# Performance work log

Hardware: AMD Instinct MI355X
Metric: run time of the kernel (lower is better)

Reference implementation:

```python
import jax, jax.numpy as jnp
import numpy as np

H_IMG, W_IMG = 32, 32   # image_size -> seq_len = 1024
NH, HD, D = 8, 32, 256  # num_heads, head_dim, d_model
B = 8


def _relative_positions(h, w):
    # Swin-style relative position index table, [h*w, h*w] int32
    y = np.arange(h); x = np.arange(w)
    coords = np.stack(np.meshgrid(y, x, indexing='ij')).reshape(2, -1)  # [2, S]
    rel = coords[:, :, None] - coords[:, None, :]                      # [2, S, S]
    rel = rel.transpose(1, 2, 0).astype(np.int64)                      # [S, S, 2]
    rel[:, :, 0] += h - 1
    rel[:, :, 1] += w - 1
    rel[:, :, 0] *= 2 * w - 1
    return np.int32(rel.sum(-1))                                       # [S, S]

_POS = _relative_positions(H_IMG, W_IMG)


def setup_inputs() -> dict:
    key = jax.random.key(0)
    ks = jax.random.split(key, 8)
    S = H_IMG * W_IMG
    return {
        'inputs_q': jax.random.normal(ks[0], (B, S, D), jnp.float32),
        'inputs_kv': jax.random.normal(ks[1], (B, S, D), jnp.float32),
        'Wq': jax.random.normal(ks[2], (D, NH, HD), jnp.float32) / np.sqrt(D),
        'bq': jnp.zeros((NH, HD), jnp.float32),
        'Wk': jax.random.normal(ks[3], (D, NH, HD), jnp.float32) / np.sqrt(D),
        'bk': jnp.zeros((NH, HD), jnp.float32),
        'Wv': jax.random.normal(ks[4], (D, NH, HD), jnp.float32) / np.sqrt(D),
        'bv': jnp.zeros((NH, HD), jnp.float32),
        'rel_table': 0.02 * jax.random.normal(ks[5], ((2 * H_IMG - 1) * (2 * W_IMG - 1), NH), jnp.float32),
        'Wo': jax.random.normal(ks[6], (NH, HD, D), jnp.float32) / np.sqrt(NH * HD),
        'bo': jnp.zeros((D,), jnp.float32),
    }


def reference(inputs_q, inputs_kv, Wq, bq, Wk, bk, Wv, bv, rel_table, Wo, bo):
    pos = jnp.asarray(_POS)                                  # [S, S] int32 (constant)
    q = jnp.einsum('bsd,dhk->bshk', inputs_q, Wq) + bq       # [B, S, H, HD]
    k = jnp.einsum('bsd,dhk->bshk', inputs_kv, Wk) + bk
    v = jnp.einsum('bsd,dhk->bshk', inputs_kv, Wv) + bv
    q = q / jnp.sqrt(jnp.asarray(HD, q.dtype))
    attn = jnp.einsum('bqhd,bkhd->bhqk', q, k)               # [B, H, S, S]
    rel_bias = rel_table[pos]                                # [S, S, H]
    attn = attn + jnp.transpose(rel_bias, (2, 0, 1))[None]   # broadcast over batch
    attn = jax.nn.softmax(attn, axis=-1)
    x = jnp.einsum('bhqk,bkhd->bqhd', attn, v)               # [B, S, H, HD]
    return jnp.einsum('bqhd,hdf->bqf', x, Wo) + bo           # [B, S, D]
```

## Files before the change

### kernel.cpp

```cpp
#include <hip/hip_runtime.h>

#define B_SZ   8
#define S_LEN  1024
#define D_MOD  256
#define NHEADS 8
#define M_ROWS 8192
#define LOG2E  1.4426950408889634f
#define QSCALE_LOG2E 0.2550352766751165f

typedef _Float16 f16x8 __attribute__((ext_vector_type(8)));
typedef _Float16 f16x4 __attribute__((ext_vector_type(4)));
typedef float    f32x4 __attribute__((ext_vector_type(4)));

__global__ __launch_bounds__(256)
void prep_kernel(const float* __restrict__ Wq, const float* __restrict__ Wk,
                 const float* __restrict__ Wv, const float* __restrict__ Wo,
                 const float* __restrict__ rel,
                 _Float16* __restrict__ wtp, float* __restrict__ tab) {
    if (blockIdx.x < 32) {
        __shared__ _Float16 Wl[32 * 264];
        const int mi = blockIdx.x >> 3;
        const int k0 = (blockIdx.x & 7) << 5;
        const float* W = (mi == 0) ? Wq : (mi == 1) ? Wk : (mi == 2) ? Wv : Wo;
        {
            const int r  = threadIdx.x >> 3;
            const int c4 = (threadIdx.x & 7) * 4;
            const float* src = W + (size_t)(k0 + r) * 256 + c4;
#pragma unroll
            for (int g = 0; g < 8; ++g) {
                f32x4 v = *(const f32x4*)(src + g * 32);
                f16x4 o;
#pragma unroll
                for (int j = 0; j < 4; ++j) o[j] = (_Float16)v[j];
                *(f16x4*)(&Wl[r * 264 + c4 + g * 32]) = o;
            }
        }
        __syncthreads();
        const int n16 = threadIdx.x >> 4;
        const int l16 = threadIdx.x & 15;
        const int kk  = k0 >> 5;
#pragma unroll
        for (int quad = 0; quad < 4; ++quad) {
            f16x8 v;
#pragma unroll
            for (int j = 0; j < 8; ++j) v[j] = Wl[(quad * 8 + j) * 264 + n16 * 16 + l16];
            *(f16x8*)(wtp + (((size_t)(mi * 16 + n16) * 8 + kk) << 9) + (quad * 16 + l16) * 8) = v;
        }
        return;
    }
    __shared__ float rl[63 * 8];
    const int dy31 = blockIdx.x - 32;
    for (int f = threadIdx.x; f < 504; f += 256) rl[f] = rel[(size_t)dy31 * 504 + f];
    __syncthreads();
    const int h  = threadIdx.x >> 5;
    const int r5 = threadIdx.x & 31;
#pragma unroll
    for (int c = 0; c < 6; ++c) {
        const int oi   = r5 * 6 + c;
        const int e    = oi >> 6;
        const int lane = oi & 63;
        const int quad = lane >> 4, l16 = lane & 15;
        f32x4 v;
#pragma unroll
        for (int reg = 0; reg < 4; ++reg) {
            const int idx = 16 * e + l16 - quad * 4 - reg + 15;
            v[reg] = rl[idx * 8 + h] * LOG2E;
        }
        *(f32x4*)(tab + (((size_t)(h * 63 + dy31) * 3 + e) << 8) + lane * 4) = v;
    }
}

__global__ __launch_bounds__(256)
void gemm_qkv_kernel(const float* __restrict__ in_q, const float* __restrict__ in_kv,
                     const _Float16* __restrict__ wtp,
                     const float* __restrict__ bq, const float* __restrict__ bk,
                     const float* __restrict__ bv,
                     _Float16* __restrict__ qs, _Float16* __restrict__ ks,
                     _Float16* __restrict__ vs) {
    __shared__ __align__(16) _Float16 As[64 * 264];
    _Float16* Ta = As;
    _Float16* Tb = As + 64 * 72;

    const int tid  = threadIdx.x;
    const int w    = tid >> 6;
    const int lane = tid & 63;
    const int quad = lane >> 4;
    const int l16  = lane & 15;
    const int m0 = blockIdx.x * 64, n0 = blockIdx.y * 64, z = blockIdx.z;
    const int b = m0 >> 10, mloc = m0 & 1023;

    {
        const int r  = tid >> 2;
        const int c4 = (tid & 3) * 4;
        const float* src = (z ? in_kv : in_q) + (size_t)(m0 + r) * 256 + c4;
        _Float16* dst = As + r * 264 + c4;
#pragma unroll
        for (int g = 0; g < 16; ++g) {
            f32x4 v = *(const f32x4*)(src + g * 16);
            f16x4 o;
#pragma unroll
            for (int j = 0; j < 4; ++j) o[j] = (_Float16)v[j];
            *(f16x4*)(dst + g * 16) = o;
        }
    }
    __syncthreads();

    const int n16base = (n0 >> 4) + (w >> 1) * 2;
    const int mA = z ? 1 : 0;
    const _Float16* wA0 = wtp + (((size_t)(mA * 16 + n16base + 0) * 8) << 9) + lane * 8;
    const _Float16* wA1 = wtp + (((size_t)(mA * 16 + n16base + 1) * 8) << 9) + lane * 8;
    const _Float16* wV0 = wtp + (((size_t)(2 * 16 + n16base + 0) * 8) << 9) + lane * 8;
    const _Float16* wV1 = wtp + (((size_t)(2 * 16 + n16base + 1) * 8) << 9) + lane * 8;
    const _Float16* arow0 = As + ((w & 1) * 32 + l16) * 264;
    const _Float16* arow1 = arow0 + 16 * 264;

    f32x4 accA[2][2], accV[2][2];
#pragma unroll
    for (int i = 0; i < 2; ++i)
#pragma unroll
        for (int j = 0; j < 2; ++j) {
            accA[i][j] = (f32x4){0.f, 0.f, 0.f, 0.f};
            accV[i][j] = (f32x4){0.f, 0.f, 0.f, 0.f};
        }

#pragma unroll
    for (int kk = 0; kk < 8; ++kk) {
        const int k8 = kk * 32 + quad * 8;
        f16x8 a0 = *(const f16x8*)(arow0 + k8);
        f16x8 a1 = *(const f16x8*)(arow1 + k8);
        f16x8 w0 = *(const f16x8*)(wA0 + kk * 512);
        f16x8 w1 = *(const f16x8*)(wA1 + kk * 512);
        accA[0][0] = __builtin_amdgcn_mfma_f32_16x16x32_f16(w0, a0, accA[0][0], 0, 0, 0);
        accA[0][1] = __builtin_amdgcn_mfma_f32_16x16x32_f16(w0, a1, accA[0][1], 0, 0, 0);
        accA[1][0] = __builtin_amdgcn_mfma_f32_16x16x32_f16(w1, a0, accA[1][0], 0, 0, 0);
        accA[1][1] = __builtin_amdgcn_mfma_f32_16x16x32_f16(w1, a1, accA[1][1], 0, 0, 0);
        if (z == 1) {
            f16x8 v0 = *(const f16x8*)(wV0 + kk * 512);
            f16x8 v1 = *(const f16x8*)(wV1 + kk * 512);
            accV[0][0] = __builtin_amdgcn_mfma_f32_16x16x32_f16(a0, v0, accV[0][0], 0, 0, 0);
            accV[0][1] = __builtin_amdgcn_mfma_f32_16x16x32_f16(a0, v1, accV[0][1], 0, 0, 0);
            accV[1][0] = __builtin_amdgcn_mfma_f32_16x16x32_f16(a1, v0, accV[1][0], 0, 0, 0);
            accV[1][1] = __builtin_amdgcn_mfma_f32_16x16x32_f16(a1, v1, accV[1][1], 0, 0, 0);
        }
    }
    __syncthreads();

    {
        const float* biasA = z ? bk : bq;
        const float  sc    = z ? 1.0f : QSCALE_LOG2E;
#pragma unroll
        for (int i = 0; i < 2; ++i) {
            f32x4 b4 = *(const f32x4*)(biasA + n0 + (w >> 1) * 32 + i * 16 + quad * 4);
#pragma unroll
            for (int jj = 0; jj < 2; ++jj) {
                f16x4 pk;
#pragma unroll
                for (int r = 0; r < 4; ++r) pk[r] = (_Float16)((accA[i][jj][r] + b4[r]) * sc);
                *(f16x4*)(Ta + ((w & 1) * 32 + jj * 16 + l16) * 72 +
                               (w >> 1) * 32 + i * 16 + quad * 4) = pk;
            }
        }
        if (z == 1) {
#pragma unroll
            for (int i = 0; i < 2; ++i) {
                const float bvv = bv[n0 + (w >> 1) * 32 + i * 16 + l16];
#pragma unroll
                for (int jj = 0; jj < 2; ++jj) {
                    f16x4 pk;
#pragma unroll
                    for (int r = 0; r < 4; ++r) pk[r] = (_Float16)(accV[jj][i][r] + bvv);
                    *(f16x4*)(Tb + ((w >> 1) * 32 + i * 16 + l16) * 72 +
                                   (w & 1) * 32 + jj * 16 + quad * 4) = pk;
                }
            }
        }
    }
    __syncthreads();
    {
        const int l16c = tid & 15, qdc = (tid >> 4) & 3;
        const int tile0 = mloc >> 5;
#pragma unroll
        for (int c2i = 0; c2i < 2; ++c2i) {
            const int c2 = w * 2 + c2i;
            const int s2 = c2 >> 2, sub = (c2 >> 1) & 1, hs = c2 & 1;
            const int bh = b * 8 + (n0 >> 5) + hs;
            const size_t dbase = (((size_t)(bh * 32 + tile0 + s2) * 2 + sub) << 9) + lane * 8;
            f16x8 va = *(const f16x8*)(Ta + (s2 * 32 + sub * 16 + l16c) * 72 +
                                            hs * 32 + qdc * 8);
            *(f16x8*)((z ? ks : qs) + dbase) = va;
            if (z == 1) {
                f16x8 vb = *(const f16x8*)(Tb + (hs * 32 + sub * 16 + l16c) * 72 +
                                                s2 * 32 + qdc * 8);
                *(f16x8*)(vs + dbase) = vb;
            }
        }
    }
}

__global__ __launch_bounds__(256)
void gemm_out_kernel(const _Float16* __restrict__ xh, const _Float16* __restrict__ wtp,
                     const float* __restrict__ bo, float* __restrict__ out) {
    __shared__ __align__(16) _Float16 As[64 * 264];
    const int tid  = threadIdx.x;
    const int w    = tid >> 6;
    const int lane = tid & 63;
    const int quad = lane >> 4;
    const int l16  = lane & 15;
    const int m0 = blockIdx.x * 64, n0 = blockIdx.y * 64;

    {
        const int r  = tid >> 2;
        const int c8 = (tid & 3) * 8;
        const _Float16* src = xh + (size_t)(m0 + r) * 256 + c8;
        _Float16* dst = As + r * 264 + c8;
#pragma unroll
        for (int g = 0; g < 8; ++g)
            *(f16x8*)(dst + g * 32) = *(const f16x8*)(src + g * 32);
    }
    __syncthreads();

    const int n16base = 48 + (n0 >> 4) + (w >> 1) * 2;
    const _Float16* w0p = wtp + (((size_t)(n16base + 0) * 8) << 9) + lane * 8;
    const _Float16* w1p = wtp + (((size_t)(n16base + 1) * 8) << 9) + lane * 8;
    const _Float16* arow0 = As + ((w & 1) * 32 + l16) * 264;
    const _Float16* arow1 = arow0 + 16 * 264;

    f32x4 acc[2][2];
#pragma unroll
    for (int i = 0; i < 2; ++i)
#pragma unroll
        for (int j = 0; j < 2; ++j) acc[i][j] = (f32x4){0.f, 0.f, 0.f, 0.f};

#pragma unroll
    for (int kk = 0; kk < 8; ++kk) {
        const int k8 = kk * 32 + quad * 8;
        f16x8 a0 = *(const f16x8*)(arow0 + k8);
        f16x8 a1 = *(const f16x8*)(arow1 + k8);
        f16x8 b0 = *(const f16x8*)(w0p + kk * 512);
        f16x8 b1 = *(const f16x8*)(w1p + kk * 512);
        acc[0][0] = __builtin_amdgcn_mfma_f32_16x16x32_f16(a0, b0, acc[0][0], 0, 0, 0);
        acc[0][1] = __builtin_amdgcn_mfma_f32_16x16x32_f16(a0, b1, acc[0][1], 0, 0, 0);
        acc[1][0] = __builtin_amdgcn_mfma_f32_16x16x32_f16(a1, b0, acc[1][0], 0, 0, 0);
        acc[1][1] = __builtin_amdgcn_mfma_f32_16x16x32_f16(a1, b1, acc[1][1], 0, 0, 0);
    }

#pragma unroll
    for (int i = 0; i < 2; ++i) {
        const int col = n0 + (w >> 1) * 32 + i * 16 + l16;
        const float bvv = bo[col];
#pragma unroll
        for (int jj = 0; jj < 2; ++jj) {
#pragma unroll
            for (int r = 0; r < 4; ++r) {
                const int row = m0 + (w & 1) * 32 + jj * 16 + quad * 4 + r;
                out[(size_t)row * 256 + col] = acc[jj][i][r] + bvv;
            }
        }
    }
}

__global__ __launch_bounds__(256)
void attn_kernel(const _Float16* __restrict__ qs, const _Float16* __restrict__ ks,
                 const _Float16* __restrict__ vs, const float* __restrict__ tab,
                 _Float16* __restrict__ xh) {
    __shared__ __align__(16) _Float16 Ps[4][32][40];

    const int tid  = threadIdx.x;
    const int w    = tid >> 6;
    const int lane = tid & 63;
    const int quad = lane >> 4;
    const int l16  = lane & 15;

    const int n     = blockIdx.x;
    const int xcd   = n & 7;
    const int local = n >> 3;
    const int bh    = xcd * 8 + (local & 7);
    const int qc    = local >> 3;
    const int b = bh >> 3, h = bh & 7;
    const int qrow_base = qc * 128 + w * 32;
    const int yq = qc * 4 + w;

    const _Float16* qp = qs + (((size_t)(bh * 32 + yq) * 2) << 9) + lane * 8;
    const f16x8 qf0 = *(const f16x8*)(qp);
    const f16x8 qf1 = *(const f16x8*)(qp + 512);
    const _Float16* kp = ks + (((size_t)bh * 64) << 9) + lane * 8;
    const _Float16* vp = vs + (((size_t)bh * 64) << 9) + lane * 8;
    const float* tb = tab + (((size_t)h * 63 * 3) << 8) + lane * 4;

    f16x8 ones;
#pragma unroll
    for (int j = 0; j < 8; ++j) ones[j] = (_Float16)1.0f;

    f32x4 o00 = {0.f,0.f,0.f,0.f}, o01 = {0.f,0.f,0.f,0.f};
    f32x4 o10 = {0.f,0.f,0.f,0.f}, o11 = {0.f,0.f,0.f,0.f};
    f32x4 ol0 = {0.f,0.f,0.f,0.f}, ol1 = {0.f,0.f,0.f,0.f};

    f16x8 kf0 = *(const f16x8*)(kp);
    f16x8 kf1 = *(const f16x8*)(kp + 512);
    f16x8 vf0 = *(const f16x8*)(vp);
    f16x8 vf1 = *(const f16x8*)(vp + 512);
    f32x4 c0 = *(const f32x4*)(tb + (yq + 31) * 768);
    f32x4 c1 = *(const f32x4*)(tb + (yq + 31) * 768 + 256);
    f32x4 c2 = *(const f32x4*)(tb + (yq + 31) * 768 + 512);

    for (int kt = 0; kt < 32; ++kt) {
        const bool more = (kt < 31);
        f16x8 nk0, nk1, nv0, nv1;
        f32x4 nc0, nc1, nc2;
        if (more) {
            const _Float16* kq = kp + (kt + 1) * 1024;
            nk0 = *(const f16x8*)(kq);
            nk1 = *(const f16x8*)(kq + 512);
            const _Float16* vq = vp + (kt + 1) * 1024;
            nv0 = *(const f16x8*)(vq);
            nv1 = *(const f16x8*)(vq + 512);
            const int d = (yq + 30 - kt) * 768;
            nc0 = *(const f32x4*)(tb + d);
            nc1 = *(const f32x4*)(tb + d + 256);
            nc2 = *(const f32x4*)(tb + d + 512);
        }

        f32x4 s00 = __builtin_amdgcn_mfma_f32_16x16x32_f16(kf0, qf0, c1, 0, 0, 0);
        f32x4 s01 = __builtin_amdgcn_mfma_f32_16x16x32_f16(kf1, qf0, c0, 0, 0, 0);
        f32x4 s10 = __builtin_amdgcn_mfma_f32_16x16x32_f16(kf0, qf1, c2, 0, 0, 0);
        f32x4 s11 = __builtin_amdgcn_mfma_f32_16x16x32_f16(kf1, qf1, c1, 0, 0, 0);

        f16x4 p;
#pragma unroll
        for (int r = 0; r < 4; ++r) p[r] = (_Float16)__builtin_amdgcn_exp2f(s00[r]);
        *(f16x4*)(&Ps[w][l16][quad * 4]) = p;
#pragma unroll
        for (int r = 0; r < 4; ++r) p[r] = (_Float16)__builtin_amdgcn_exp2f(s01[r]);
        *(f16x4*)(&Ps[w][l16][16 + quad * 4]) = p;
#pragma unroll
        for (int r = 0; r < 4; ++r) p[r] = (_Float16)__builtin_amdgcn_exp2f(s10[r]);
        *(f16x4*)(&Ps[w][16 + l16][quad * 4]) = p;
#pragma unroll
        for (int r = 0; r < 4; ++r) p[r] = (_Float16)__builtin_amdgcn_exp2f(s11[r]);
        *(f16x4*)(&Ps[w][16 + l16][16 + quad * 4]) = p;

        const f16x8 pf0 = *(const f16x8*)(&Ps[w][l16][quad * 8]);
        const f16x8 pf1 = *(const f16x8*)(&Ps[w][16 + l16][quad * 8]);
        o00 = __builtin_amdgcn_mfma_f32_16x16x32_f16(vf0, pf0, o00, 0, 0, 0);
        o01 = __builtin_amdgcn_mfma_f32_16x16x32_f16(vf0, pf1, o01, 0, 0, 0);
        o10 = __builtin_amdgcn_mfma_f32_16x16x32_f16(vf1, pf0, o10, 0, 0, 0);
        o11 = __builtin_amdgcn_mfma_f32_16x16x32_f16(vf1, pf1, o11, 0, 0, 0);
        ol0 = __builtin_amdgcn_mfma_f32_16x16x32_f16(ones, pf0, ol0, 0, 0, 0);
        ol1 = __builtin_amdgcn_mfma_f32_16x16x32_f16(ones, pf1, ol1, 0, 0, 0);

        if (more) {
            kf0 = nk0; kf1 = nk1; vf0 = nv0; vf1 = nv1;
            c0 = nc0; c1 = nc1; c2 = nc2;
        }
    }

#pragma unroll
    for (int qh = 0; qh < 2; ++qh) {
        const f32x4 onl = qh ? o01 : o00;
        const f32x4 onh = qh ? o11 : o10;
        const f32x4 ll  = qh ? ol1 : ol0;
        const float inv = __builtin_amdgcn_rcpf(ll[0]);
        const int qg = qrow_base + qh * 16 + l16;
        f16x4 u, v;
#pragma unroll
        for (int r = 0; r < 4; ++r) {
            u[r] = (_Float16)(onl[r] * inv);
            v[r] = (_Float16)(onh[r] * inv);
        }
        _Float16* op = xh + ((size_t)(b * S_LEN + qg)) * D_MOD + h * 32 + quad * 4;
        *(f16x4*)(op)      = u;
        *(f16x4*)(op + 16) = v;
    }
}

extern "C" void kernel_launch(void* const* d_in, const int* in_sizes, int n_in,
                              void* d_out, int out_size, void* d_ws, size_t ws_size,
                              hipStream_t stream) {
    const float* in_q  = (const float*)d_in[0];
    const float* in_kv = (const float*)d_in[1];
    const float* Wq    = (const float*)d_in[2];
    const float* bq    = (const float*)d_in[3];
    const float* Wk    = (const float*)d_in[4];
    const float* bk    = (const float*)d_in[5];
    const float* Wv    = (const float*)d_in[6];
    const float* bv    = (const float*)d_in[7];
    const float* rel   = (const float*)d_in[8];
    const float* Wo    = (const float*)d_in[9];
    const float* bo    = (const float*)d_in[10];
    float* out = (float*)d_out;

    char* wsb = (char*)d_ws;
    _Float16* qs  = (_Float16*)(wsb);
    _Float16* ks  = (_Float16*)(wsb + (size_t)4  * 1048576);
    _Float16* vs  = (_Float16*)(wsb + (size_t)8  * 1048576);
    _Float16* xh  = (_Float16*)(wsb + (size_t)12 * 1048576);
    _Float16* wtp = (_Float16*)(wsb + (size_t)16 * 1048576);
    float*    tab = (float*)   (wsb + (size_t)17 * 1048576);

    const dim3 blk(256);

    prep_kernel<<<dim3(95), blk, 0, stream>>>(Wq, Wk, Wv, Wo, rel, wtp, tab);
    gemm_qkv_kernel<<<dim3(128, 4, 2), blk, 0, stream>>>(
        in_q, in_kv, wtp, bq, bk, bv, qs, ks, vs);
    attn_kernel<<<dim3(512), blk, 0, stream>>>(qs, ks, vs, tab, xh);
    gemm_out_kernel<<<dim3(128, 4), blk, 0, stream>>>(xh, wtp, bo, out);
}
```

Baseline: 124.1 us.

## Widen QKV GEMM tiles, double attention queries per wave, fragment-layout attention output

```diff
diff --git a/kernel.cpp b/kernel.cpp
--- a/kernel.cpp
+++ b/kernel.cpp
@@ -4,7 +4,6 @@
 #define S_LEN  1024
 #define D_MOD  256
 #define NHEADS 8
-#define M_ROWS 8192
 #define LOG2E  1.4426950408889634f
 #define QSCALE_LOG2E 0.2550352766751165f
 
@@ -77,23 +76,20 @@
                      const float* __restrict__ bv,
                      _Float16* __restrict__ qs, _Float16* __restrict__ ks,
                      _Float16* __restrict__ vs) {
-    __shared__ __align__(16) _Float16 As[64 * 264];
-    _Float16* Ta = As;
-    _Float16* Tb = As + 64 * 72;
-
+    __shared__ __align__(16) _Float16 Lds[256 * 72];
     const int tid  = threadIdx.x;
     const int w    = tid >> 6;
     const int lane = tid & 63;
     const int quad = lane >> 4;
     const int l16  = lane & 15;
-    const int m0 = blockIdx.x * 64, n0 = blockIdx.y * 64, z = blockIdx.z;
+    const int m0 = blockIdx.x * 64, z = blockIdx.y;
     const int b = m0 >> 10, mloc = m0 & 1023;
 
     {
         const int r  = tid >> 2;
         const int c4 = (tid & 3) * 4;
         const float* src = (z ? in_kv : in_q) + (size_t)(m0 + r) * 256 + c4;
-        _Float16* dst = As + r * 264 + c4;
+        _Float16* dst = Lds + r * 264 + c4;
 #pragma unroll
         for (int g = 0; g < 16; ++g) {
             f32x4 v = *(const f32x4*)(src + g * 16);
@@ -105,42 +101,38 @@
     }
     __syncthreads();
 
-    const int n16base = (n0 >> 4) + (w >> 1) * 2;
-    const int mA = z ? 1 : 0;
-    const _Float16* wA0 = wtp + (((size_t)(mA * 16 + n16base + 0) * 8) << 9) + lane * 8;
-    const _Float16* wA1 = wtp + (((size_t)(mA * 16 + n16base + 1) * 8) << 9) + lane * 8;
-    const _Float16* wV0 = wtp + (((size_t)(2 * 16 + n16base + 0) * 8) << 9) + lane * 8;
-    const _Float16* wV1 = wtp + (((size_t)(2 * 16 + n16base + 1) * 8) << 9) + lane * 8;
-    const _Float16* arow0 = As + ((w & 1) * 32 + l16) * 264;
-    const _Float16* arow1 = arow0 + 16 * 264;
-
-    f32x4 accA[2][2], accV[2][2];
-#pragma unroll
-    for (int i = 0; i < 2; ++i)
-#pragma unroll
-        for (int j = 0; j < 2; ++j) {
-            accA[i][j] = (f32x4){0.f, 0.f, 0.f, 0.f};
-            accV[i][j] = (f32x4){0.f, 0.f, 0.f, 0.f};
-        }
-
+    f32x4 accA[4][4], accV[4][4];
+#pragma unroll
+    for (int i = 0; i < 4; ++i)
+#pragma unroll
+        for (int j = 0; j < 4; ++j) {
+            accA[j][i] = (f32x4){0.f, 0.f, 0.f, 0.f};
+            accV[j][i] = (f32x4){0.f, 0.f, 0.f, 0.f};
+        }
+
+    const int mA = z;
 #pragma unroll
     for (int kk = 0; kk < 8; ++kk) {
         const int k8 = kk * 32 + quad * 8;
-        f16x8 a0 = *(const f16x8*)(arow0 + k8);
-        f16x8 a1 = *(const f16x8*)(arow1 + k8);
-        f16x8 w0 = *(const f16x8*)(wA0 + kk * 512);
-        f16x8 w1 = *(const f16x8*)(wA1 + kk * 512);
-        accA[0][0] = __builtin_amdgcn_mfma_f32_16x16x32_f16(w0, a0, accA[0][0], 0, 0, 0);
-        accA[0][1] = __builtin_amdgcn_mfma_f32_16x16x32_f16(w0, a1, accA[0][1], 0, 0, 0);
-        accA[1][0] = __builtin_amdgcn_mfma_f32_16x16x32_f16(w1, a0, accA[1][0], 0, 0, 0);
-        accA[1][1] = __builtin_amdgcn_mfma_f32_16x16x32_f16(w1, a1, accA[1][1], 0, 0, 0);
+        f16x8 a[4];
+#pragma unroll
+        for (int jj = 0; jj < 4; ++jj)
+            a[jj] = *(const f16x8*)(Lds + (16 * jj + l16) * 264 + k8);
+#pragma unroll
+        for (int i = 0; i < 4; ++i) {
+            f16x8 wa = *(const f16x8*)(wtp + (((size_t)(mA * 16 + w * 4 + i) * 8 + kk) << 9) + lane * 8);
+#pragma unroll
+            for (int jj = 0; jj < 4; ++jj)
+                accA[jj][i] = __builtin_amdgcn_mfma_f32_16x16x32_f16(wa, a[jj], accA[jj][i], 0, 0, 0);
+        }
         if (z == 1) {
-            f16x8 v0 = *(const f16x8*)(wV0 + kk * 512);
-            f16x8 v1 = *(const f16x8*)(wV1 + kk * 512);
-            accV[0][0] = __builtin_amdgcn_mfma_f32_16x16x32_f16(a0, v0, accV[0][0], 0, 0, 0);
-            accV[0][1] = __builtin_amdgcn_mfma_f32_16x16x32_f16(a0, v1, accV[0][1], 0, 0, 0);
-            accV[1][0] = __builtin_amdgcn_mfma_f32_16x16x32_f16(a1, v0, accV[1][0], 0, 0, 0);
-            accV[1][1] = __builtin_amdgcn_mfma_f32_16x16x32_f16(a1, v1, accV[1][1], 0, 0, 0);
+#pragma unroll
+            for (int i = 0; i < 4; ++i) {
+                f16x8 wv = *(const f16x8*)(wtp + (((size_t)(32 + w * 4 + i) * 8 + kk) << 9) + lane * 8);
+#pragma unroll
+                for (int jj = 0; jj < 4; ++jj)
+                    accV[jj][i] = __builtin_amdgcn_mfma_f32_16x16x32_f16(a[jj], wv, accV[jj][i], 0, 0, 0);
+            }
         }
     }
     __syncthreads();
@@ -149,81 +141,65 @@
         const float* biasA = z ? bk : bq;
         const float  sc    = z ? 1.0f : QSCALE_LOG2E;
 #pragma unroll
-        for (int i = 0; i < 2; ++i) {
-            f32x4 b4 = *(const f32x4*)(biasA + n0 + (w >> 1) * 32 + i * 16 + quad * 4);
-#pragma unroll
-            for (int jj = 0; jj < 2; ++jj) {
+        for (int i = 0; i < 4; ++i) {
+            f32x4 b4 = *(const f32x4*)(biasA + (w * 4 + i) * 16 + quad * 4);
+#pragma unroll
+            for (int jj = 0; jj < 4; ++jj) {
                 f16x4 pk;
 #pragma unroll
-                for (int r = 0; r < 4; ++r) pk[r] = (_Float16)((accA[i][jj][r] + b4[r]) * sc);
-                *(f16x4*)(Ta + ((w & 1) * 32 + jj * 16 + l16) * 72 +
-                               (w >> 1) * 32 + i * 16 + quad * 4) = pk;
-            }
-        }
-        if (z == 1) {
-#pragma unroll
-            for (int i = 0; i < 2; ++i) {
-                const float bvv = bv[n0 + (w >> 1) * 32 + i * 16 + l16];
-#pragma unroll
-                for (int jj = 0; jj < 2; ++jj) {
-                    f16x4 pk;
-#pragma unroll
-                    for (int r = 0; r < 4; ++r) pk[r] = (_Float16)(accV[jj][i][r] + bvv);
-                    *(f16x4*)(Tb + ((w >> 1) * 32 + i * 16 + l16) * 72 +
-                                   (w & 1) * 32 + jj * 16 + quad * 4) = pk;
-                }
+                for (int r = 0; r < 4; ++r) pk[r] = (_Float16)((accA[jj][i][r] + b4[r]) * sc);
+                *(f16x4*)(Lds + (16 * jj + l16) * 264 + (w * 4 + i) * 16 + quad * 4) = pk;
             }
         }
     }
     __syncthreads();
     {
-        const int l16c = tid & 15, qdc = (tid >> 4) & 3;
-        const int tile0 = mloc >> 5;
-#pragma unroll
-        for (int c2i = 0; c2i < 2; ++c2i) {
-            const int c2 = w * 2 + c2i;
-            const int s2 = c2 >> 2, sub = (c2 >> 1) & 1, hs = c2 & 1;
-            const int bh = b * 8 + (n0 >> 5) + hs;
-            const size_t dbase = (((size_t)(bh * 32 + tile0 + s2) * 2 + sub) << 9) + lane * 8;
-            f16x8 va = *(const f16x8*)(Ta + (s2 * 32 + sub * 16 + l16c) * 72 +
-                                            hs * 32 + qdc * 8);
-            *(f16x8*)((z ? ks : qs) + dbase) = va;
-            if (z == 1) {
-                f16x8 vb = *(const f16x8*)(Tb + (hs * 32 + sub * 16 + l16c) * 72 +
-                                                s2 * 32 + qdc * 8);
-                *(f16x8*)(vs + dbase) = vb;
-            }
+        _Float16* dstm = z ? ks : qs;
+#pragma unroll
+        for (int c = 0; c < 8; ++c) {
+            const int sg  = w * 8 + c;
+            const int tl  = sg >> 4, sub = (sg >> 3) & 1, h = sg & 7;
+            f16x8 v = *(const f16x8*)(Lds + (tl * 32 + sub * 16 + l16) * 264 + h * 32 + quad * 8);
+            const int tg = (mloc >> 5) + tl;
+            *(f16x8*)(dstm + ((((size_t)(b * 8 + h) * 32 + tg) * 2 + sub) << 9) + lane * 8) = v;
+        }
+    }
+    if (z == 1) {
+        __syncthreads();
+#pragma unroll
+        for (int i = 0; i < 4; ++i) {
+            const float bvv = bv[(w * 4 + i) * 16 + l16];
+#pragma unroll
+            for (int jj = 0; jj < 4; ++jj) {
+                f16x4 pk;
+#pragma unroll
+                for (int r = 0; r < 4; ++r) pk[r] = (_Float16)(accV[jj][i][r] + bvv);
+                *(f16x4*)(Lds + ((w * 4 + i) * 16 + l16) * 72 + 16 * jj + quad * 4) = pk;
+            }
+        }
+        __syncthreads();
+#pragma unroll
+        for (int c = 0; c < 8; ++c) {
+            const int sg  = w * 8 + c;
+            const int h = sg & 7, tl = (sg >> 3) & 1, sub = (sg >> 4) & 1;
+            f16x8 v = *(const f16x8*)(Lds + (h * 32 + sub * 16 + l16) * 72 + tl * 32 + quad * 8);
+            const int tg = (mloc >> 5) + tl;
+            *(f16x8*)(vs + ((((size_t)(b * 8 + h) * 32 + tg) * 2 + sub) << 9) + lane * 8) = v;
         }
     }
 }
 
 __global__ __launch_bounds__(256)
-void gemm_out_kernel(const _Float16* __restrict__ xh, const _Float16* __restrict__ wtp,
+void gemm_out_kernel(const _Float16* __restrict__ xs, const _Float16* __restrict__ wtp,
                      const float* __restrict__ bo, float* __restrict__ out) {
-    __shared__ __align__(16) _Float16 As[64 * 264];
     const int tid  = threadIdx.x;
     const int w    = tid >> 6;
     const int lane = tid & 63;
     const int quad = lane >> 4;
     const int l16  = lane & 15;
-    const int m0 = blockIdx.x * 64, n0 = blockIdx.y * 64;
-
-    {
-        const int r  = tid >> 2;
-        const int c8 = (tid & 3) * 8;
-        const _Float16* src = xh + (size_t)(m0 + r) * 256 + c8;
-        _Float16* dst = As + r * 264 + c8;
-#pragma unroll
-        for (int g = 0; g < 8; ++g)
-            *(f16x8*)(dst + g * 32) = *(const f16x8*)(src + g * 32);
-    }
-    __syncthreads();
-
-    const int n16base = 48 + (n0 >> 4) + (w >> 1) * 2;
-    const _Float16* w0p = wtp + (((size_t)(n16base + 0) * 8) << 9) + lane * 8;
-    const _Float16* w1p = wtp + (((size_t)(n16base + 1) * 8) << 9) + lane * 8;
-    const _Float16* arow0 = As + ((w & 1) * 32 + l16) * 264;
-    const _Float16* arow1 = arow0 + 16 * 264;
+    const int bx = blockIdx.x, by = blockIdx.y;
+    const int mt0  = bx * 4 + (w & 1) * 2;
+    const int n16a = by * 4 + (w >> 1) * 2;
 
     f32x4 acc[2][2];
 #pragma unroll
@@ -233,11 +209,10 @@
 
 #pragma unroll
     for (int kk = 0; kk < 8; ++kk) {
-        const int k8 = kk * 32 + quad * 8;
-        f16x8 a0 = *(const f16x8*)(arow0 + k8);
-        f16x8 a1 = *(const f16x8*)(arow1 + k8);
-        f16x8 b0 = *(const f16x8*)(w0p + kk * 512);
-        f16x8 b1 = *(const f16x8*)(w1p + kk * 512);
+        f16x8 a0 = *(const f16x8*)(xs + (((size_t)(mt0 + 0) * 8 + kk) << 9) + lane * 8);
+        f16x8 a1 = *(const f16x8*)(xs + (((size_t)(mt0 + 1) * 8 + kk) << 9) + lane * 8);
+        f16x8 b0 = *(const f16x8*)(wtp + (((size_t)(48 + n16a + 0) * 8 + kk) << 9) + lane * 8);
+        f16x8 b1 = *(const f16x8*)(wtp + (((size_t)(48 + n16a + 1) * 8 + kk) << 9) + lane * 8);
         acc[0][0] = __builtin_amdgcn_mfma_f32_16x16x32_f16(a0, b0, acc[0][0], 0, 0, 0);
         acc[0][1] = __builtin_amdgcn_mfma_f32_16x16x32_f16(a0, b1, acc[0][1], 0, 0, 0);
         acc[1][0] = __builtin_amdgcn_mfma_f32_16x16x32_f16(a1, b0, acc[1][0], 0, 0, 0);
@@ -246,13 +221,13 @@
 
 #pragma unroll
     for (int i = 0; i < 2; ++i) {
-        const int col = n0 + (w >> 1) * 32 + i * 16 + l16;
+        const int col = (n16a + i) * 16 + l16;
         const float bvv = bo[col];
 #pragma unroll
         for (int jj = 0; jj < 2; ++jj) {
 #pragma unroll
             for (int r = 0; r < 4; ++r) {
-                const int row = m0 + (w & 1) * 32 + jj * 16 + quad * 4 + r;
+                const int row = (mt0 + jj) * 16 + quad * 4 + r;
                 out[(size_t)row * 256 + col] = acc[jj][i][r] + bvv;
             }
         }
@@ -262,8 +237,8 @@
 __global__ __launch_bounds__(256)
 void attn_kernel(const _Float16* __restrict__ qs, const _Float16* __restrict__ ks,
                  const _Float16* __restrict__ vs, const float* __restrict__ tab,
-                 _Float16* __restrict__ xh) {
-    __shared__ __align__(16) _Float16 Ps[4][32][40];
+                 _Float16* __restrict__ xs) {
+    __shared__ __align__(16) _Float16 Ps[4][64][40];
 
     const int tid  = threadIdx.x;
     const int w    = tid >> 6;
@@ -277,36 +252,47 @@
     const int bh    = xcd * 8 + (local & 7);
     const int qc    = local >> 3;
     const int b = bh >> 3, h = bh & 7;
-    const int qrow_base = qc * 128 + w * 32;
-    const int yq = qc * 4 + w;
-
-    const _Float16* qp = qs + (((size_t)(bh * 32 + yq) * 2) << 9) + lane * 8;
-    const f16x8 qf0 = *(const f16x8*)(qp);
-    const f16x8 qf1 = *(const f16x8*)(qp + 512);
+    const int y1 = qc * 8 + w * 2;
+
+    const _Float16* qbase = qs + (((size_t)(bh * 32 + y1) * 2) << 9) + lane * 8;
+    f16x8 qf[4];
+    qf[0] = *(const f16x8*)(qbase);
+    qf[1] = *(const f16x8*)(qbase + 512);
+    qf[2] = *(const f16x8*)(qbase + 1024);
+    qf[3] = *(const f16x8*)(qbase + 1536);
+
     const _Float16* kp = ks + (((size_t)bh * 64) << 9) + lane * 8;
     const _Float16* vp = vs + (((size_t)bh * 64) << 9) + lane * 8;
-    const float* tb = tab + (((size_t)h * 63 * 3) << 8) + lane * 4;
+    const float* tb = tab + (((size_t)h * 189) << 8) + lane * 4;
 
     f16x8 ones;
 #pragma unroll
     for (int j = 0; j < 8; ++j) ones[j] = (_Float16)1.0f;
 
-    f32x4 o00 = {0.f,0.f,0.f,0.f}, o01 = {0.f,0.f,0.f,0.f};
-    f32x4 o10 = {0.f,0.f,0.f,0.f}, o11 = {0.f,0.f,0.f,0.f};
-    f32x4 ol0 = {0.f,0.f,0.f,0.f}, ol1 = {0.f,0.f,0.f,0.f};
+    f32x4 o[2][4], ol[4];
+#pragma unroll
+    for (int j = 0; j < 4; ++j) {
+        o[0][j] = (f32x4){0.f, 0.f, 0.f, 0.f};
+        o[1][j] = (f32x4){0.f, 0.f, 0.f, 0.f};
+        ol[j]   = (f32x4){0.f, 0.f, 0.f, 0.f};
+    }
 
     f16x8 kf0 = *(const f16x8*)(kp);
     f16x8 kf1 = *(const f16x8*)(kp + 512);
     f16x8 vf0 = *(const f16x8*)(vp);
     f16x8 vf1 = *(const f16x8*)(vp + 512);
-    f32x4 c0 = *(const f32x4*)(tb + (yq + 31) * 768);
-    f32x4 c1 = *(const f32x4*)(tb + (yq + 31) * 768 + 256);
-    f32x4 c2 = *(const f32x4*)(tb + (yq + 31) * 768 + 512);
-
+    f32x4 cy1[3], cy2[3];
+#pragma unroll
+    for (int e = 0; e < 3; ++e) {
+        cy1[e] = *(const f32x4*)(tb + (((y1 + 31) * 3 + e) << 8));
+        cy2[e] = *(const f32x4*)(tb + (((y1 + 32) * 3 + e) << 8));
+    }
+
+#pragma unroll 2
     for (int kt = 0; kt < 32; ++kt) {
         const bool more = (kt < 31);
         f16x8 nk0, nk1, nv0, nv1;
-        f32x4 nc0, nc1, nc2;
+        f32x4 nc[3];
         if (more) {
             const _Float16* kq = kp + (kt + 1) * 1024;
             nk0 = *(const f16x8*)(kq);
@@ -314,62 +300,59 @@
             const _Float16* vq = vp + (kt + 1) * 1024;
             nv0 = *(const f16x8*)(vq);
             nv1 = *(const f16x8*)(vq + 512);
-            const int d = (yq + 30 - kt) * 768;
-            nc0 = *(const f32x4*)(tb + d);
-            nc1 = *(const f32x4*)(tb + d + 256);
-            nc2 = *(const f32x4*)(tb + d + 512);
-        }
-
-        f32x4 s00 = __builtin_amdgcn_mfma_f32_16x16x32_f16(kf0, qf0, c1, 0, 0, 0);
-        f32x4 s01 = __builtin_amdgcn_mfma_f32_16x16x32_f16(kf1, qf0, c0, 0, 0, 0);
-        f32x4 s10 = __builtin_amdgcn_mfma_f32_16x16x32_f16(kf0, qf1, c2, 0, 0, 0);
-        f32x4 s11 = __builtin_amdgcn_mfma_f32_16x16x32_f16(kf1, qf1, c1, 0, 0, 0);
-
+            const int d = (y1 + 30 - kt) * 3;
+#pragma unroll
+            for (int e = 0; e < 3; ++e) nc[e] = *(const f32x4*)(tb + ((d + e) << 8));
+        }
+
+        f32x4 s;
         f16x4 p;
-#pragma unroll
-        for (int r = 0; r < 4; ++r) p[r] = (_Float16)__builtin_amdgcn_exp2f(s00[r]);
-        *(f16x4*)(&Ps[w][l16][quad * 4]) = p;
-#pragma unroll
-        for (int r = 0; r < 4; ++r) p[r] = (_Float16)__builtin_amdgcn_exp2f(s01[r]);
-        *(f16x4*)(&Ps[w][l16][16 + quad * 4]) = p;
-#pragma unroll
-        for (int r = 0; r < 4; ++r) p[r] = (_Float16)__builtin_amdgcn_exp2f(s10[r]);
-        *(f16x4*)(&Ps[w][16 + l16][quad * 4]) = p;
-#pragma unroll
-        for (int r = 0; r < 4; ++r) p[r] = (_Float16)__builtin_amdgcn_exp2f(s11[r]);
-        *(f16x4*)(&Ps[w][16 + l16][16 + quad * 4]) = p;
-
-        const f16x8 pf0 = *(const f16x8*)(&Ps[w][l16][quad * 8]);
-        const f16x8 pf1 = *(const f16x8*)(&Ps[w][16 + l16][quad * 8]);
-        o00 = __builtin_amdgcn_mfma_f32_16x16x32_f16(vf0, pf0, o00, 0, 0, 0);
-        o01 = __builtin_amdgcn_mfma_f32_16x16x32_f16(vf0, pf1, o01, 0, 0, 0);
-        o10 = __builtin_amdgcn_mfma_f32_16x16x32_f16(vf1, pf0, o10, 0, 0, 0);
-        o11 = __builtin_amdgcn_mfma_f32_16x16x32_f16(vf1, pf1, o11, 0, 0, 0);
-        ol0 = __builtin_amdgcn_mfma_f32_16x16x32_f16(ones, pf0, ol0, 0, 0, 0);
-        ol1 = __builtin_amdgcn_mfma_f32_16x16x32_f16(ones, pf1, ol1, 0, 0, 0);
+        _Float16* pw;
+#pragma unroll
+        for (int j = 0; j < 4; ++j) {
+            const f32x4* cy = (j < 2) ? cy1 : cy2;
+            pw = &Ps[w][16 * j + l16][quad * 4];
+            s = __builtin_amdgcn_mfma_f32_16x16x32_f16(kf0, qf[j], cy[(j & 1) + 1], 0, 0, 0);
+#pragma unroll
+            for (int r = 0; r < 4; ++r) p[r] = (_Float16)__builtin_amdgcn_exp2f(s[r]);
+            *(f16x4*)(pw) = p;
+            s = __builtin_amdgcn_mfma_f32_16x16x32_f16(kf1, qf[j], cy[(j & 1)], 0, 0, 0);
+#pragma unroll
+            for (int r = 0; r < 4; ++r) p[r] = (_Float16)__builtin_amdgcn_exp2f(s[r]);
+            *(f16x4*)(pw + 16) = p;
+        }
+
+#pragma unroll
+        for (int j = 0; j < 4; ++j) {
+            const f16x8 pf = *(const f16x8*)(&Ps[w][16 * j + l16][quad * 8]);
+            o[0][j] = __builtin_amdgcn_mfma_f32_16x16x32_f16(vf0, pf, o[0][j], 0, 0, 0);
+            o[1][j] = __builtin_amdgcn_mfma_f32_16x16x32_f16(vf1, pf, o[1][j], 0, 0, 0);
+            ol[j]   = __builtin_amdgcn_mfma_f32_16x16x32_f16(ones, pf, ol[j], 0, 0, 0);
+        }
 
         if (more) {
             kf0 = nk0; kf1 = nk1; vf0 = nv0; vf1 = nv1;
-            c0 = nc0; c1 = nc1; c2 = nc2;
-        }
-    }
-
-#pragma unroll
-    for (int qh = 0; qh < 2; ++qh) {
-        const f32x4 onl = qh ? o01 : o00;
-        const f32x4 onh = qh ? o11 : o10;
-        const f32x4 ll  = qh ? ol1 : ol0;
-        const float inv = __builtin_amdgcn_rcpf(ll[0]);
-        const int qg = qrow_base + qh * 16 + l16;
-        f16x4 u, v;
-#pragma unroll
-        for (int r = 0; r < 4; ++r) {
-            u[r] = (_Float16)(onl[r] * inv);
-            v[r] = (_Float16)(onh[r] * inv);
-        }
-        _Float16* op = xh + ((size_t)(b * S_LEN + qg)) * D_MOD + h * 32 + quad * 4;
-        *(f16x4*)(op)      = u;
-        *(f16x4*)(op + 16) = v;
+#pragma unroll
+            for (int e = 0; e < 3; ++e) { cy2[e] = cy1[e]; cy1[e] = nc[e]; }
+        }
+    }
+
+#pragma unroll
+    for (int j = 0; j < 4; ++j) {
+        const float inv = __builtin_amdgcn_rcpf(ol[j][0]);
+#pragma unroll
+        for (int i = 0; i < 2; ++i) {
+            f16x4 pk;
+#pragma unroll
+            for (int r = 0; r < 4; ++r) pk[r] = (_Float16)(o[i][j][r] * inv);
+            *(f16x4*)(&Ps[w][16 * j + l16][16 * i + quad * 4]) = pk;
+        }
+    }
+    const int mt0 = b * 64 + qc * 16 + w * 4;
+#pragma unroll
+    for (int s4 = 0; s4 < 4; ++s4) {
+        f16x8 af = *(const f16x8*)(&Ps[w][16 * s4 + l16][quad * 8]);
+        *(f16x8*)(xs + (((size_t)(mt0 + s4) * 8 + h) << 9) + lane * 8) = af;
     }
 }
 
@@ -393,15 +376,15 @@
     _Float16* qs  = (_Float16*)(wsb);
     _Float16* ks  = (_Float16*)(wsb + (size_t)4  * 1048576);
     _Float16* vs  = (_Float16*)(wsb + (size_t)8  * 1048576);
-    _Float16* xh  = (_Float16*)(wsb + (size_t)12 * 1048576);
+    _Float16* xs  = (_Float16*)(wsb + (size_t)12 * 1048576);
     _Float16* wtp = (_Float16*)(wsb + (size_t)16 * 1048576);
     float*    tab = (float*)   (wsb + (size_t)17 * 1048576);
 
     const dim3 blk(256);
 
     prep_kernel<<<dim3(95), blk, 0, stream>>>(Wq, Wk, Wv, Wo, rel, wtp, tab);
-    gemm_qkv_kernel<<<dim3(128, 4, 2), blk, 0, stream>>>(
+    gemm_qkv_kernel<<<dim3(128, 2), blk, 0, stream>>>(
         in_q, in_kv, wtp, bq, bk, bv, qs, ks, vs);
-    attn_kernel<<<dim3(512), blk, 0, stream>>>(qs, ks, vs, tab, xh);
-    gemm_out_kernel<<<dim3(128, 4), blk, 0, stream>>>(xh, wtp, bo, out);
-}
+    attn_kernel<<<dim3(256), blk, 0, stream>>>(qs, ks, vs, tab, xs);
+    gemm_out_kernel<<<dim3(128, 4), blk, 0, stream>>>(xs, wtp, bo, out);
+}
```

Result: slower. 129.0 us (+4.0%).
